# Optimization experiments

Measured on AMD Instinct MI355X. Metric: run time of the kernel, lower is better.

## Reference

```python
import jax, jax.numpy as jnp
import numpy as np

C = 256
B, H, W = 16, 64, 64
CQK = C // 8


def setup_inputs() -> dict:
    key = jax.random.key(0)
    ks = jax.random.split(key, 8)
    s = 0.02
    return {
        "x": jax.random.normal(ks[0], (B, C, H, W), dtype=jnp.float32),
        "Wq": jax.random.normal(ks[1], (CQK, C), dtype=jnp.float32) * s,
        "bq": jax.random.normal(ks[2], (CQK,), dtype=jnp.float32) * s,
        "Wk": jax.random.normal(ks[3], (CQK, C), dtype=jnp.float32) * s,
        "bk": jax.random.normal(ks[4], (CQK,), dtype=jnp.float32) * s,
        "Wv": jax.random.normal(ks[5], (C, C), dtype=jnp.float32) * s,
        "bv": jax.random.normal(ks[6], (C,), dtype=jnp.float32) * s,
        "gamma": jax.random.normal(ks[7], (1,), dtype=jnp.float32) * 0.1,
    }


def reference(x, Wq, bq, Wk, bk, Wv, bv, gamma):
    b, c, h, w = x.shape
    n = h * w
    xf = x.reshape(b, c, n)  # flatten spatial -> tokens
    # 1x1 convs are per-token linear maps over channels
    q = jnp.einsum('oc,bcn->bon', Wq, xf) + bq[None, :, None]  # [B, C/8, N]
    k = jnp.einsum('oc,bcn->bon', Wk, xf) + bk[None, :, None]  # [B, C/8, N]
    v = jnp.einsum('oc,bcn->bon', Wv, xf) + bv[None, :, None]  # [B, C,   N]
    attn = jnp.einsum('bdi,bdj->bij', q, k)        # [B, N, N] = Q^T K
    attn = jax.nn.softmax(attn, axis=2)            # softmax over keys
    out = jnp.einsum('bcj,bij->bci', v, attn)      # V @ attn^T -> [B, C, N]
    out = out.reshape(b, c, h, w)
    return gamma[0] * out + x
```

## Files before the change

kernel.cpp:

```cpp
#include <hip/hip_runtime.h>
#include <hip/hip_bf16.h>

#define BB   16
#define CCH  256
#define DQK  32
#define NTOK 4096

typedef __attribute__((ext_vector_type(8)))  short short8;
typedef __attribute__((ext_vector_type(4)))  float f32x4;
typedef __attribute__((ext_vector_type(16))) float f32x16;
typedef unsigned short u16t;
typedef unsigned int   u32t;

__device__ __forceinline__ u16t f2bf(float f){
  u32t u = __builtin_bit_cast(u32t, f);
  u += 0x7FFFu + ((u >> 16) & 1u);
  return (u16t)(u >> 16);
}
__device__ __forceinline__ u32t pk2(float a, float b){
  return (u32t)f2bf(a) | ((u32t)f2bf(b) << 16);
}
__device__ __forceinline__ u32t cvtpk(float lo, float hi_){
  u32t d;
  asm("v_cvt_pk_bf16_f32 %0, %1, %2" : "=v"(d) : "v"(lo), "v"(hi_));
  return d;
}
__device__ __forceinline__ void lane32swap(u32t& a, u32t& b){
  asm("v_permlane32_swap_b32 %0, %1" : "+v"(a), "+v"(b));
}
__device__ __forceinline__ float swapadd(float x){
  u32t a = __builtin_bit_cast(u32t, x), b = a;
  lane32swap(a, b);
  return __builtin_bit_cast(float, a) + __builtin_bit_cast(float, b);
}
__device__ __forceinline__ void gload16(const void* g, void* l){
  __builtin_amdgcn_global_load_lds(
      (const __attribute__((address_space(1))) void*)g,
      (__attribute__((address_space(3))) void*)l, 16, 0, 0);
}
__device__ __forceinline__ f32x16 zero16(){
  f32x16 z;
  #pragma unroll
  for (int i = 0; i < 16; ++i) z[i] = 0.f;
  return z;
}
#define mfma32(A, B, C) __builtin_amdgcn_mfma_f32_32x32x16_bf16((A), (B), (C), 0, 0, 0)

__global__ __launch_bounds__(256) void k_wconv(const float* __restrict__ Wq,
    const float* __restrict__ Wk, const float* __restrict__ Wv,
    u16t* __restrict__ o){
  const int base = (blockIdx.x * 256 + threadIdx.x) * 4;
  float4 v;
  if (base < 8192)        v = *(const float4*)(Wq + base);
  else if (base < 16384)  v = *(const float4*)(Wk + base - 8192);
  else                    v = *(const float4*)(Wv + base - 16384);
  *(uint2*)(o + base) = make_uint2(pk2(v.x, v.y), pk2(v.z, v.w));
}

__global__ __launch_bounds__(256) void k_proj(const float* __restrict__ x,
    const u16t* __restrict__ Wb,
    const float* __restrict__ bq, const float* __restrict__ bk,
    const float* __restrict__ bv,
    u16t* __restrict__ Q, u16t* __restrict__ K, u16t* __restrict__ V){
  __shared__ __align__(16) u16t xt[32 * 512];
  const int b = blockIdx.y, nb = blockIdx.x * 64;
  const int tid = threadIdx.x;
  const int w = tid >> 6, lane = tid & 63;
  const int lo = lane & 15, g = lane >> 4;

  const float* xb = x + (size_t)b * CCH * NTOK + nb;
  const int cg = tid >> 4, n0 = (tid & 15) * 4;
  #pragma unroll
  for (int rep = 0; rep < 16; ++rep){
    const int c = rep * 16 + cg;
    float4 v = *(const float4*)(xb + (size_t)c * NTOK + n0);
    const int chunkb = (n0 >> 4) * 8 + (c >> 5);
    const int fl = 16 * ((c >> 3) & 3);
    const int e = c & 7;
    xt[chunkb * 512 + ((n0 & 15) + 0 + fl) * 8 + e] = f2bf(v.x);
    xt[chunkb * 512 + ((n0 & 15) + 1 + fl) * 8 + e] = f2bf(v.y);
    xt[chunkb * 512 + ((n0 & 15) + 2 + fl) * 8 + e] = f2bf(v.z);
    xt[chunkb * 512 + ((n0 & 15) + 3 + fl) * 8 + e] = f2bf(v.w);
  }
  __syncthreads();

  #pragma unroll
  for (int ot = 0; ot < 5; ++ot){
    const u16t* Wrow; const float* bias; int ob; int mode;
    if (ot == 0){
      if (w < 2){ Wrow = Wb;        bias = bq; ob = w * 16;       mode = 0; }
      else      { Wrow = Wb + 8192; bias = bk; ob = (w - 2) * 16; mode = 1; }
    } else { Wrow = Wb + 16384; bias = bv; ob = (ot - 1) * 64 + w * 16; mode = 2; }
    const u16t* wp = Wrow + (size_t)(ob + lo) * CCH + g * 8;

    f32x4 acc[4];
    #pragma unroll
    for (int s = 0; s < 4; ++s) acc[s] = (f32x4){0.f, 0.f, 0.f, 0.f};
    #pragma unroll
    for (int kc = 0; kc < CCH; kc += 32){
      const short8 af = *(const short8*)(wp + kc);
      #pragma unroll
      for (int s = 0; s < 4; ++s){
        const short8 bf = *(const short8*)(xt + (s * 8 + (kc >> 5)) * 512 + lane * 8);
        acc[s] = __builtin_amdgcn_mfma_f32_16x16x32_bf16(af, bf, acc[s], 0, 0, 0);
      }
    }
    #pragma unroll
    for (int s = 0; s < 4; ++s){
      #pragma unroll
      for (int r = 0; r < 4; ++r){
        const int o = ob + 4 * g + r;
        const int n = nb + s * 16 + lo;
        float val = acc[s][r] + bias[o];
        if (mode == 0) val *= 1.44269504088896f;
        const u16t h = f2bf(val);
        if (mode == 0)      Q[((size_t)b * NTOK + n) * DQK + o] = h;
        else if (mode == 1) K[((size_t)b * NTOK + n) * DQK + o] = h;
        else                V[((size_t)b * CCH + o) * NTOK + n] = h;
      }
    }
  }
}

__global__ __launch_bounds__(256, 2) void k_attn(
    const u16t* __restrict__ Q, const u16t* __restrict__ K, const u16t* __restrict__ V,
    const float* __restrict__ x, const float* __restrict__ gamma,
    float* __restrict__ out){
  __shared__ __align__(16) u16t KT[2 * 2048];
  __shared__ __align__(16) u16t Vt[2][CCH * 64];
  const int bid = blockIdx.x;
  const int b  = ((bid & 7) << 1) | ((bid >> 3) & 1);
  const int qt = bid >> 4;
  const int tid = threadIdx.x, w = tid >> 6, lane = tid & 63;
  const int ql = lane & 31, hi = lane >> 5;
  const int qg = qt * 128 + w * 32;

  const u16t* Qb = Q + (size_t)b * NTOK * DQK;
  const u16t* Kb = K + (size_t)b * NTOK * DQK;
  const u16t* Vb = V + (size_t)b * CCH * NTOK;

  const short8 qf0 = *(const short8*)(Qb + (size_t)(qg + ql) * DQK + hi * 8);
  const short8 qf1 = *(const short8*)(Qb + (size_t)(qg + ql) * DQK + 16 + hi * 8);

  f32x16 acc[8];
  #pragma unroll
  for (int c = 0; c < 8; ++c) acc[c] = zero16();
  float l = 0.f;

  const int vrow0 = w * 64 + (lane >> 3);
  const int jsrc  = ((lane & 7) ^ (lane >> 3)) * 8;
  const char* vsrc0 = (const char*)Vb + ((size_t)vrow0 * NTOK + jsrc) * 2;
  const size_t kse = (size_t)((w & 1) * 32 + ql) * DQK + (w >> 1) * 16 + hi * 8;
  const char* ksrc0 = (const char*)Kb + kse * 2;
  const int kla = lane * 16;
  int vaddA[4], vaddB[4];
  #pragma unroll
  for (int kt = 0; kt < 4; ++kt){
    vaddA[kt] = ql * 128 + (((kt * 2 + hi) ^ (ql & 7)) * 16);
    vaddB[kt] = vaddA[kt] + 32768;
  }
  const char* ldsV = (const char*)&Vt[0][0];
  const char* ldsK = (const char*)&KT[0];
  u32t pf[4][4];

  #define PACK_PF(S0, S1) \
    { _Pragma("unroll") \
      for (int js = 0; js < 2; ++js){ \
        _Pragma("unroll") \
        for (int t2 = 0; t2 < 2; ++t2){ \
          const int kt_ = js * 2 + t2, bo = 8 * t2; \
          u32t A1, A2, B1, B2; \
          if (js == 0){ \
            A1 = cvtpk(S0[bo+0], S0[bo+1]); A2 = cvtpk(S0[bo+2], S0[bo+3]); \
            B1 = cvtpk(S0[bo+4], S0[bo+5]); B2 = cvtpk(S0[bo+6], S0[bo+7]); \
          } else { \
            A1 = cvtpk(S1[bo+0], S1[bo+1]); A2 = cvtpk(S1[bo+2], S1[bo+3]); \
            B1 = cvtpk(S1[bo+4], S1[bo+5]); B2 = cvtpk(S1[bo+6], S1[bo+7]); \
          } \
          lane32swap(A1, B1); lane32swap(A2, B2); \
          pf[kt_][0] = A1; pf[kt_][1] = A2; pf[kt_][2] = B1; pf[kt_][3] = B2; \
        } } }

  #define QK_STEP(KRD, S0, S1) \
    { const char* kb_ = ldsK + (KRD) * 4096; \
      const short8 kf00 = *(const short8*)(kb_ + kla + 0 * 1024); \
      const short8 kf10 = *(const short8*)(kb_ + kla + 1 * 1024); \
      const short8 kf01 = *(const short8*)(kb_ + kla + 2 * 1024); \
      const short8 kf11 = *(const short8*)(kb_ + kla + 3 * 1024); \
      S0 = mfma32(kf00, qf0, zero16()); S0 = mfma32(kf01, qf1, S0); \
      S1 = mfma32(kf10, qf0, zero16()); S1 = mfma32(kf11, qf1, S1); }

  #define ESL(S, B) \
    { S[(B)+0] = __builtin_amdgcn_exp2f(S[(B)+0]); r0 += S[(B)+0]; \
      S[(B)+1] = __builtin_amdgcn_exp2f(S[(B)+1]); r1 += S[(B)+1]; \
      S[(B)+2] = __builtin_amdgcn_exp2f(S[(B)+2]); r2 += S[(B)+2]; \
      S[(B)+3] = __builtin_amdgcn_exp2f(S[(B)+3]); r3 += S[(B)+3]; }

  #define PVCHUNK(CS, VRD, EXPSLICE) \
    { const short8 vf0 = *(const short8*)(ldsV + ((VRD)?vaddB[0]:vaddA[0]) + (CS)*4096); \
      const short8 vf1 = *(const short8*)(ldsV + ((VRD)?vaddB[1]:vaddA[1]) + (CS)*4096); \
      const short8 vf2 = *(const short8*)(ldsV + ((VRD)?vaddB[2]:vaddA[2]) + (CS)*4096); \
      const short8 vf3 = *(const short8*)(ldsV + ((VRD)?vaddB[3]:vaddA[3]) + (CS)*4096); \
      acc[CS] = mfma32(vf0, pb0, acc[CS]); \
      acc[CS] = mfma32(vf1, pb1, acc[CS]); \
      acc[CS] = mfma32(vf2, pb2, acc[CS]); \
      acc[CS] = mfma32(vf3, pb3, acc[CS]); \
      EXPSLICE \
      __builtin_amdgcn_sched_group_barrier(0x100, 4, 0); \
      __builtin_amdgcn_sched_group_barrier(0x8,   4, 0); \
      __builtin_amdgcn_sched_group_barrier(0x2,  10, 0); }

  #define NOSL

  #define ABODY(T, VRD, KRD, KST) { \
      const int t128_ = ((T) + 1) * 128; \
      _Pragma("unroll") \
      for (int i = 0; i < 8; ++i) \
        gload16(vsrc0 + (size_t)i * 65536 + t128_, &Vt[(VRD)^1][w * 4096 + i * 512]); \
      { const int kt2_ = ((T) + 2 <= 63) ? (T) + 2 : 63; \
        gload16(ksrc0 + (size_t)kt2_ * 4096, &KT[(KST) * 2048 + w * 512]); } \
      f32x16 s0, s1; \
      QK_STEP(KRD, s0, s1); \
      const short8 pb0 = __builtin_bit_cast(short8, make_uint4(pf[0][0], pf[0][1], pf[0][2], pf[0][3])); \
      const short8 pb1 = __builtin_bit_cast(short8, make_uint4(pf[1][0], pf[1][1], pf[1][2], pf[1][3])); \
      const short8 pb2 = __builtin_bit_cast(short8, make_uint4(pf[2][0], pf[2][1], pf[2][2], pf[2][3])); \
      const short8 pb3 = __builtin_bit_cast(short8, make_uint4(pf[3][0], pf[3][1], pf[3][2], pf[3][3])); \
      float r0 = 0.f, r1 = 0.f, r2 = 0.f, r3 = 0.f; \
      PVCHUNK(0, VRD, ESL(s0, 0)) \
      PVCHUNK(1, VRD, ESL(s0, 4)) \
      PVCHUNK(2, VRD, ESL(s0, 8)) \
      PVCHUNK(3, VRD, ESL(s0, 12)) \
      PVCHUNK(4, VRD, ESL(s1, 0)) \
      PVCHUNK(5, VRD, ESL(s1, 4)) \
      PVCHUNK(6, VRD, ESL(s1, 8)) \
      PVCHUNK(7, VRD, ESL(s1, 12)) \
      l += (r0 + r1) + (r2 + r3); \
      PACK_PF(s0, s1); \
      __syncthreads(); }

  #pragma unroll
  for (int i = 0; i < 8; ++i)
    gload16(vsrc0 + (size_t)i * 65536, &Vt[0][w * 4096 + i * 512]);
  gload16(ksrc0,        &KT[0 * 2048 + w * 512]);
  gload16(ksrc0 + 4096, &KT[1 * 2048 + w * 512]);
  __syncthreads();

  {
    f32x16 s0, s1;
    QK_STEP(0, s0, s1);
    float r0 = 0.f, r1 = 0.f, r2 = 0.f, r3 = 0.f;
    ESL(s0, 0) ESL(s0, 4) ESL(s0, 8) ESL(s0, 12)
    ESL(s1, 0) ESL(s1, 4) ESL(s1, 8) ESL(s1, 12)
    l = (r0 + r1) + (r2 + r3);
    PACK_PF(s0, s1);
  }
  __syncthreads();

  for (int t = 0; t < 62; t += 2){
    ABODY(t,     0, 1, 0)
    ABODY(t + 1, 1, 0, 1)
  }
  ABODY(62, 0, 1, 0)

  {
    const short8 pb0 = __builtin_bit_cast(short8, make_uint4(pf[0][0], pf[0][1], pf[0][2], pf[0][3]));
    const short8 pb1 = __builtin_bit_cast(short8, make_uint4(pf[1][0], pf[1][1], pf[1][2], pf[1][3]));
    const short8 pb2 = __builtin_bit_cast(short8, make_uint4(pf[2][0], pf[2][1], pf[2][2], pf[2][3]));
    const short8 pb3 = __builtin_bit_cast(short8, make_uint4(pf[3][0], pf[3][1], pf[3][2], pf[3][3]));
    PVCHUNK(0, 1, NOSL) PVCHUNK(1, 1, NOSL) PVCHUNK(2, 1, NOSL) PVCHUNK(3, 1, NOSL)
    PVCHUNK(4, 1, NOSL) PVCHUNK(5, 1, NOSL) PVCHUNK(6, 1, NOSL) PVCHUNK(7, 1, NOSL)
  }

  const float lfull = swapadd(l);
  const float inv = 1.0f / lfull;
  const float gm = gamma[0];
  const int n = qg + ql;
  #pragma unroll
  for (int cs = 0; cs < 8; ++cs){
    #pragma unroll
    for (int r = 0; r < 16; ++r){
      const int c = cs * 32 + (r & 3) + 8 * (r >> 2) + 4 * hi;
      const size_t idx = ((size_t)b * CCH + c) * NTOK + n;
      out[idx] = gm * (acc[cs][r] * inv) + x[idx];
    }
  }
  #undef PACK_PF
  #undef QK_STEP
  #undef ESL
  #undef PVCHUNK
  #undef NOSL
  #undef ABODY
}

extern "C" void kernel_launch(void* const* d_in, const int* in_sizes, int n_in,
                              void* d_out, int out_size, void* d_ws, size_t ws_size,
                              hipStream_t stream) {
  const float* x     = (const float*)d_in[0];
  const float* Wq    = (const float*)d_in[1];
  const float* bq    = (const float*)d_in[2];
  const float* Wk    = (const float*)d_in[3];
  const float* bk    = (const float*)d_in[4];
  const float* Wv    = (const float*)d_in[5];
  const float* bv    = (const float*)d_in[6];
  const float* gamma = (const float*)d_in[7];
  float* out = (float*)d_out;

  char* ws = (char*)d_ws;
  u16t* Qw = (u16t*)(ws);
  u16t* Kw = (u16t*)(ws + 4194304);
  u16t* Vw = (u16t*)(ws + 8388608);
  u16t* Wbf = (u16t*)d_out;

  hipLaunchKernelGGL(k_wconv, dim3(80), dim3(256), 0, stream, Wq, Wk, Wv, Wbf);
  hipLaunchKernelGGL(k_proj, dim3(NTOK / 64, BB), dim3(256), 0, stream,
                     x, Wbf, bq, bk, bv, Qw, Kw, Vw);
  hipLaunchKernelGGL(k_attn, dim3(512), dim3(256), 0, stream,
                     Qw, Kw, Vw, x, gamma, out);
}
```

Before: 191.4 us.

## Use FP8 for V and probabilities in the PV matmul

The projection kernel now writes V as FP8 in a pre-swizzled layout, and the softmax probabilities are packed to FP8. The PV product then runs on fp8 32x32x16 MFMAs instead of bf16. This halves V global traffic and LDS footprint and uses the fp8 matrix path. The cost is lower precision in both V and the attention weights, which may exceed accuracy tolerance, along with new swizzle and packing logic.

```diff
diff --git a/kernel.cpp b/kernel.cpp
--- a/kernel.cpp
+++ b/kernel.cpp
@@ -11,6 +11,7 @@
 typedef __attribute__((ext_vector_type(16))) float f32x16;
 typedef unsigned short u16t;
 typedef unsigned int   u32t;
+typedef long long      i64t;
 
 __device__ __forceinline__ u16t f2bf(float f){
   u32t u = __builtin_bit_cast(u32t, f);
@@ -20,11 +21,6 @@
 __device__ __forceinline__ u32t pk2(float a, float b){
   return (u32t)f2bf(a) | ((u32t)f2bf(b) << 16);
 }
-__device__ __forceinline__ u32t cvtpk(float lo, float hi_){
-  u32t d;
-  asm("v_cvt_pk_bf16_f32 %0, %1, %2" : "=v"(d) : "v"(lo), "v"(hi_));
-  return d;
-}
 __device__ __forceinline__ void lane32swap(u32t& a, u32t& b){
   asm("v_permlane32_swap_b32 %0, %1" : "+v"(a), "+v"(b));
 }
@@ -44,7 +40,16 @@
   for (int i = 0; i < 16; ++i) z[i] = 0.f;
   return z;
 }
-#define mfma32(A, B, C) __builtin_amdgcn_mfma_f32_32x32x16_bf16((A), (B), (C), 0, 0, 0)
+#define mfma32(A, B, C)  __builtin_amdgcn_mfma_f32_32x32x16_bf16((A), (B), (C), 0, 0, 0)
+#define mfma8(A, B, C)   __builtin_amdgcn_mfma_f32_32x32x16_fp8_fp8((A), (B), (C), 0, 0, 0)
+__device__ __forceinline__ u32t pack4fp8(float a, float b, float c, float d){
+  int t = __builtin_amdgcn_cvt_pk_fp8_f32(a, b, 0, false);
+  t = __builtin_amdgcn_cvt_pk_fp8_f32(c, d, t, true);
+  return (u32t)t;
+}
+__device__ __forceinline__ unsigned char tofp8(float v){
+  return (unsigned char)(__builtin_amdgcn_cvt_pk_fp8_f32(v, 0.f, 0, false) & 0xFF);
+}
 
 __global__ __launch_bounds__(256) void k_wconv(const float* __restrict__ Wq,
     const float* __restrict__ Wk, const float* __restrict__ Wv,
@@ -61,7 +66,7 @@
     const u16t* __restrict__ Wb,
     const float* __restrict__ bq, const float* __restrict__ bk,
     const float* __restrict__ bv,
-    u16t* __restrict__ Q, u16t* __restrict__ K, u16t* __restrict__ V){
+    u16t* __restrict__ Q, u16t* __restrict__ K, unsigned char* __restrict__ V){
   __shared__ __align__(16) u16t xt[32 * 512];
   const int b = blockIdx.y, nb = blockIdx.x * 64;
   const int tid = threadIdx.x;
@@ -112,22 +117,27 @@
         const int o = ob + 4 * g + r;
         const int n = nb + s * 16 + lo;
         float val = acc[s][r] + bias[o];
-        if (mode == 0) val *= 1.44269504088896f;
-        const u16t h = f2bf(val);
-        if (mode == 0)      Q[((size_t)b * NTOK + n) * DQK + o] = h;
-        else if (mode == 1) K[((size_t)b * NTOK + n) * DQK + o] = h;
-        else                V[((size_t)b * CCH + o) * NTOK + n] = h;
+        if (mode == 0){
+          val *= 1.44269504088896f;
+          Q[((size_t)b * NTOK + n) * DQK + o] = f2bf(val);
+        } else if (mode == 1){
+          K[((size_t)b * NTOK + n) * DQK + o] = f2bf(val);
+        } else {
+          const int swz = ((((s * 2) + (lo >> 3)) ^ ((o >> 1) & 7)) << 3) + (lo & 7);
+          V[((size_t)b * CCH + o) * (size_t)NTOK + nb + swz] = tofp8(val);
+        }
       }
     }
   }
 }
 
 __global__ __launch_bounds__(256, 2) void k_attn(
-    const u16t* __restrict__ Q, const u16t* __restrict__ K, const u16t* __restrict__ V,
+    const u16t* __restrict__ Q, const u16t* __restrict__ K,
+    const unsigned char* __restrict__ V,
     const float* __restrict__ x, const float* __restrict__ gamma,
     float* __restrict__ out){
   __shared__ __align__(16) u16t KT[2 * 2048];
-  __shared__ __align__(16) u16t Vt[2][CCH * 64];
+  __shared__ __align__(16) unsigned char Vt[2][16384];
   const int bid = blockIdx.x;
   const int b  = ((bid & 7) << 1) | ((bid >> 3) & 1);
   const int qt = bid >> 4;
@@ -137,7 +147,7 @@
 
   const u16t* Qb = Q + (size_t)b * NTOK * DQK;
   const u16t* Kb = K + (size_t)b * NTOK * DQK;
-  const u16t* Vb = V + (size_t)b * CCH * NTOK;
+  const unsigned char* Vb = V + (size_t)b * CCH * NTOK;
 
   const short8 qf0 = *(const short8*)(Qb + (size_t)(qg + ql) * DQK + hi * 8);
   const short8 qf1 = *(const short8*)(Qb + (size_t)(qg + ql) * DQK + 16 + hi * 8);
@@ -147,39 +157,35 @@
   for (int c = 0; c < 8; ++c) acc[c] = zero16();
   float l = 0.f;
 
-  const int vrow0 = w * 64 + (lane >> 3);
-  const int jsrc  = ((lane & 7) ^ (lane >> 3)) * 8;
-  const char* vsrc0 = (const char*)Vb + ((size_t)vrow0 * NTOK + jsrc) * 2;
+  const char* vsrc0 = (const char*)Vb + (size_t)(w * 64 + (lane >> 2)) * NTOK + (lane & 3) * 16;
   const size_t kse = (size_t)((w & 1) * 32 + ql) * DQK + (w >> 1) * 16 + hi * 8;
   const char* ksrc0 = (const char*)Kb + kse * 2;
   const int kla = lane * 16;
   int vaddA[4], vaddB[4];
   #pragma unroll
   for (int kt = 0; kt < 4; ++kt){
-    vaddA[kt] = ql * 128 + (((kt * 2 + hi) ^ (ql & 7)) * 16);
-    vaddB[kt] = vaddA[kt] + 32768;
+    vaddA[kt] = ql * 64 + (((kt * 2 + hi) ^ ((ql >> 1) & 7)) << 3);
+    vaddB[kt] = vaddA[kt] + 16384;
   }
   const char* ldsV = (const char*)&Vt[0][0];
   const char* ldsK = (const char*)&KT[0];
-  u32t pf[4][4];
-
-  #define PACK_PF(S0, S1) \
+  u32t pf2[4][2];
+
+  #define PACK_PF8(S0, S1) \
     { _Pragma("unroll") \
-      for (int js = 0; js < 2; ++js){ \
-        _Pragma("unroll") \
-        for (int t2 = 0; t2 < 2; ++t2){ \
-          const int kt_ = js * 2 + t2, bo = 8 * t2; \
-          u32t A1, A2, B1, B2; \
-          if (js == 0){ \
-            A1 = cvtpk(S0[bo+0], S0[bo+1]); A2 = cvtpk(S0[bo+2], S0[bo+3]); \
-            B1 = cvtpk(S0[bo+4], S0[bo+5]); B2 = cvtpk(S0[bo+6], S0[bo+7]); \
-          } else { \
-            A1 = cvtpk(S1[bo+0], S1[bo+1]); A2 = cvtpk(S1[bo+2], S1[bo+3]); \
-            B1 = cvtpk(S1[bo+4], S1[bo+5]); B2 = cvtpk(S1[bo+6], S1[bo+7]); \
-          } \
-          lane32swap(A1, B1); lane32swap(A2, B2); \
-          pf[kt_][0] = A1; pf[kt_][1] = A2; pf[kt_][2] = B1; pf[kt_][3] = B2; \
-        } } }
+      for (int kt_ = 0; kt_ < 4; ++kt_){ \
+        const int bo = (kt_ & 1) * 8; \
+        u32t A, B; \
+        if (kt_ < 2){ \
+          A = pack4fp8(S0[bo+0], S0[bo+1], S0[bo+2], S0[bo+3]); \
+          B = pack4fp8(S0[bo+4], S0[bo+5], S0[bo+6], S0[bo+7]); \
+        } else { \
+          A = pack4fp8(S1[bo+0], S1[bo+1], S1[bo+2], S1[bo+3]); \
+          B = pack4fp8(S1[bo+4], S1[bo+5], S1[bo+6], S1[bo+7]); \
+        } \
+        lane32swap(A, B); \
+        pf2[kt_][0] = A; pf2[kt_][1] = B; \
+      } }
 
   #define QK_STEP(KRD, S0, S1) \
     { const char* kb_ = ldsK + (KRD) * 4096; \
@@ -197,34 +203,36 @@
       S[(B)+3] = __builtin_amdgcn_exp2f(S[(B)+3]); r3 += S[(B)+3]; }
 
   #define PVCHUNK(CS, VRD, EXPSLICE) \
-    { const short8 vf0 = *(const short8*)(ldsV + ((VRD)?vaddB[0]:vaddA[0]) + (CS)*4096); \
-      const short8 vf1 = *(const short8*)(ldsV + ((VRD)?vaddB[1]:vaddA[1]) + (CS)*4096); \
-      const short8 vf2 = *(const short8*)(ldsV + ((VRD)?vaddB[2]:vaddA[2]) + (CS)*4096); \
-      const short8 vf3 = *(const short8*)(ldsV + ((VRD)?vaddB[3]:vaddA[3]) + (CS)*4096); \
-      acc[CS] = mfma32(vf0, pb0, acc[CS]); \
-      acc[CS] = mfma32(vf1, pb1, acc[CS]); \
-      acc[CS] = mfma32(vf2, pb2, acc[CS]); \
-      acc[CS] = mfma32(vf3, pb3, acc[CS]); \
+    { const i64t vf0 = *(const i64t*)(ldsV + ((VRD)?vaddB[0]:vaddA[0]) + (CS)*2048); \
+      const i64t vf1 = *(const i64t*)(ldsV + ((VRD)?vaddB[1]:vaddA[1]) + (CS)*2048); \
+      const i64t vf2 = *(const i64t*)(ldsV + ((VRD)?vaddB[2]:vaddA[2]) + (CS)*2048); \
+      const i64t vf3 = *(const i64t*)(ldsV + ((VRD)?vaddB[3]:vaddA[3]) + (CS)*2048); \
+      acc[CS] = mfma8(vf0, pb0, acc[CS]); \
+      acc[CS] = mfma8(vf1, pb1, acc[CS]); \
+      acc[CS] = mfma8(vf2, pb2, acc[CS]); \
+      acc[CS] = mfma8(vf3, pb3, acc[CS]); \
       EXPSLICE \
       __builtin_amdgcn_sched_group_barrier(0x100, 4, 0); \
       __builtin_amdgcn_sched_group_barrier(0x8,   4, 0); \
       __builtin_amdgcn_sched_group_barrier(0x2,  10, 0); }
 
   #define NOSL
+  #define PBDEFS \
+      const i64t pb0 = __builtin_bit_cast(i64t, make_uint2(pf2[0][0], pf2[0][1])); \
+      const i64t pb1 = __builtin_bit_cast(i64t, make_uint2(pf2[1][0], pf2[1][1])); \
+      const i64t pb2 = __builtin_bit_cast(i64t, make_uint2(pf2[2][0], pf2[2][1])); \
+      const i64t pb3 = __builtin_bit_cast(i64t, make_uint2(pf2[3][0], pf2[3][1]));
 
   #define ABODY(T, VRD, KRD, KST) { \
-      const int t128_ = ((T) + 1) * 128; \
+      const int toff_ = ((T) + 1) * 64; \
       _Pragma("unroll") \
-      for (int i = 0; i < 8; ++i) \
-        gload16(vsrc0 + (size_t)i * 65536 + t128_, &Vt[(VRD)^1][w * 4096 + i * 512]); \
+      for (int i = 0; i < 4; ++i) \
+        gload16(vsrc0 + (size_t)i * 16 * NTOK + toff_, &Vt[(VRD)^1][w * 4096 + i * 1024]); \
       { const int kt2_ = ((T) + 2 <= 63) ? (T) + 2 : 63; \
         gload16(ksrc0 + (size_t)kt2_ * 4096, &KT[(KST) * 2048 + w * 512]); } \
       f32x16 s0, s1; \
       QK_STEP(KRD, s0, s1); \
-      const short8 pb0 = __builtin_bit_cast(short8, make_uint4(pf[0][0], pf[0][1], pf[0][2], pf[0][3])); \
-      const short8 pb1 = __builtin_bit_cast(short8, make_uint4(pf[1][0], pf[1][1], pf[1][2], pf[1][3])); \
-      const short8 pb2 = __builtin_bit_cast(short8, make_uint4(pf[2][0], pf[2][1], pf[2][2], pf[2][3])); \
-      const short8 pb3 = __builtin_bit_cast(short8, make_uint4(pf[3][0], pf[3][1], pf[3][2], pf[3][3])); \
+      PBDEFS \
       float r0 = 0.f, r1 = 0.f, r2 = 0.f, r3 = 0.f; \
       PVCHUNK(0, VRD, ESL(s0, 0)) \
       PVCHUNK(1, VRD, ESL(s0, 4)) \
@@ -235,12 +243,12 @@
       PVCHUNK(6, VRD, ESL(s1, 8)) \
       PVCHUNK(7, VRD, ESL(s1, 12)) \
       l += (r0 + r1) + (r2 + r3); \
-      PACK_PF(s0, s1); \
+      PACK_PF8(s0, s1); \
       __syncthreads(); }
 
   #pragma unroll
-  for (int i = 0; i < 8; ++i)
-    gload16(vsrc0 + (size_t)i * 65536, &Vt[0][w * 4096 + i * 512]);
+  for (int i = 0; i < 4; ++i)
+    gload16(vsrc0 + (size_t)i * 16 * NTOK, &Vt[0][w * 4096 + i * 1024]);
   gload16(ksrc0,        &KT[0 * 2048 + w * 512]);
   gload16(ksrc0 + 4096, &KT[1 * 2048 + w * 512]);
   __syncthreads();
@@ -252,7 +260,7 @@
     ESL(s0, 0) ESL(s0, 4) ESL(s0, 8) ESL(s0, 12)
     ESL(s1, 0) ESL(s1, 4) ESL(s1, 8) ESL(s1, 12)
     l = (r0 + r1) + (r2 + r3);
-    PACK_PF(s0, s1);
+    PACK_PF8(s0, s1);
   }
   __syncthreads();
 
@@ -263,10 +271,7 @@
   ABODY(62, 0, 1, 0)
 
   {
-    const short8 pb0 = __builtin_bit_cast(short8, make_uint4(pf[0][0], pf[0][1], pf[0][2], pf[0][3]));
-    const short8 pb1 = __builtin_bit_cast(short8, make_uint4(pf[1][0], pf[1][1], pf[1][2], pf[1][3]));
-    const short8 pb2 = __builtin_bit_cast(short8, make_uint4(pf[2][0], pf[2][1], pf[2][2], pf[2][3]));
-    const short8 pb3 = __builtin_bit_cast(short8, make_uint4(pf[3][0], pf[3][1], pf[3][2], pf[3][3]));
+    PBDEFS
     PVCHUNK(0, 1, NOSL) PVCHUNK(1, 1, NOSL) PVCHUNK(2, 1, NOSL) PVCHUNK(3, 1, NOSL)
     PVCHUNK(4, 1, NOSL) PVCHUNK(5, 1, NOSL) PVCHUNK(6, 1, NOSL) PVCHUNK(7, 1, NOSL)
   }
@@ -284,11 +289,12 @@
       out[idx] = gm * (acc[cs][r] * inv) + x[idx];
     }
   }
-  #undef PACK_PF
+  #undef PACK_PF8
   #undef QK_STEP
   #undef ESL
   #undef PVCHUNK
   #undef NOSL
+  #undef PBDEFS
   #undef ABODY
 }
 
@@ -308,7 +314,7 @@
   char* ws = (char*)d_ws;
   u16t* Qw = (u16t*)(ws);
   u16t* Kw = (u16t*)(ws + 4194304);
-  u16t* Vw = (u16t*)(ws + 8388608);
+  unsigned char* Vw = (unsigned char*)(ws + 8388608);
   u16t* Wbf = (u16t*)d_out;
 
   hipLaunchKernelGGL(k_wconv, dim3(80), dim3(256), 0, stream, Wq, Wk, Wv, Wbf);
```

Result: faster. 168.3 us (-12.1%).
